# Kernel optimization log

Measured on AMD Instinct MI355X. Metric: run time of the kernel, lower is better.

## Reference

```python
import jax, jax.numpy as jnp
import numpy as np

B = 64          # graphs in batch
NVARS = 256     # variables per graph
LITS_PER = 2 * NVARS
NL = B * LITS_PER      # 32768 literals
CLS_PER = 1024
NC = B * CLS_PER       # 65536 clauses
K = 3                  # literals per clause (3-CNF)
D = 128
NUM_ITERS = 8


def setup_inputs() -> dict:
    key = jax.random.key(0)
    ks = jax.random.split(key, 16)
    # edge list of the sparse clause-literal incidence matrix adj_t [NC, NL]
    edge_clause = jnp.repeat(jnp.arange(NC, dtype=jnp.int32), K)            # [E]
    clause_graph = jnp.repeat(jnp.arange(NC, dtype=jnp.int32) // CLS_PER, K)
    lit_local = jax.random.randint(ks[0], (NC * K,), 0, LITS_PER, dtype=jnp.int32)
    edge_lit = clause_graph * LITS_PER + lit_local                          # [E]
    s = 0.05
    inp = {
        "edge_clause": edge_clause,
        "edge_lit": edge_lit,
        "x_l0": jax.random.uniform(ks[1], (NL, D), jnp.float32),
        "x_c0": jax.random.uniform(ks[2], (NC, D), jnp.float32),
        "W_ih_lc": jax.random.normal(ks[3], (D, D), jnp.float32) * s,
        "W_hh_lc": jax.random.normal(ks[4], (D, D), jnp.float32) * s,
        "b_ih_lc": jax.random.normal(ks[5], (D,), jnp.float32) * s,
        "b_hh_lc": jax.random.normal(ks[6], (D,), jnp.float32) * s,
        "W_ih_cl": jax.random.normal(ks[7], (D, 2 * D), jnp.float32) * s,
        "W_hh_cl": jax.random.normal(ks[8], (D, D), jnp.float32) * s,
        "b_ih_cl": jax.random.normal(ks[9], (D,), jnp.float32) * s,
        "b_hh_cl": jax.random.normal(ks[10], (D,), jnp.float32) * s,
        "L_vote_w": jax.random.normal(ks[11], (1, D), jnp.float32) * s,
        "L_vote_b": jax.random.normal(ks[12], (1,), jnp.float32) * s,
        "true_vec_w": jax.random.normal(ks[13], (1, D), jnp.float32) * s,
        "num_iters": NUM_ITERS,
    }
    return inp


def _l2norm(x):
    return x / jnp.linalg.norm(x, axis=1, keepdims=True)


def _rnn_cell(x, h, Wih, Whh, bih, bhh):
    # torch nn.RNN (tanh) single step: h' = tanh(x W_ih^T + b_ih + h W_hh^T + b_hh)
    return jnp.tanh(x @ Wih.T + bih + h @ Whh.T + bhh)


def _flip(x_l):
    # per graph, swap [pos vars | neg vars] halves
    return x_l.reshape(B, 2, NVARS, D)[:, ::-1].reshape(NL, D)


def reference(edge_clause, edge_lit, x_l0, x_c0,
              W_ih_lc, W_hh_lc, b_ih_lc, b_hh_lc,
              W_ih_cl, W_hh_cl, b_ih_cl, b_hh_cl,
              L_vote_w, L_vote_b, true_vec_w, num_iters):
    x_l = _l2norm(x_l0)
    x_c = _l2norm(x_c0)

    truth0 = x_l @ true_vec_w.T          # [NL, 1]
    clause0 = x_c                        # [NC, D]

    def step(carry, _):
        x_l, x_c = carry
        # LC: clause messages = adj_t @ x_l  (sparse matmul as gather+segment_sum)
        msg_c = jax.ops.segment_sum(x_l[edge_lit], edge_clause, num_segments=NC)
        x_c_new = _rnn_cell(msg_c, x_c, W_ih_lc, W_hh_lc, b_ih_lc, b_hh_lc)
        # CL: literal messages = adj_t^T @ x_c_new
        msg_l = jax.ops.segment_sum(x_c_new[edge_clause], edge_lit, num_segments=NL)
        inp = jnp.concatenate([msg_l, _flip(x_l)], axis=1)   # [NL, 2D]
        x_l_new = _rnn_cell(inp, x_l, W_ih_cl, W_hh_cl, b_ih_cl, b_hh_cl)
        x_l_n = _l2norm(x_l_new)
        x_c_n = _l2norm(x_c_new)
        truth = x_l_n @ true_vec_w.T                          # [NL, 1]
        return (x_l_n, x_c_n), (truth, x_c_n)

    (x_l, x_c), (truths, clauses) = jax.lax.scan(step, (x_l, x_c), None, length=num_iters)

    truth_all = jnp.concatenate([truth0[None], truths], axis=0)    # [T+1, NL, 1]
    clause_all = jnp.concatenate([clause0[None], clauses], axis=0)  # [T+1, NC, D]

    x_l_vote = x_l @ L_vote_w.T + L_vote_b                   # [NL, 1]
    vote_mean_pool = x_l_vote.reshape(B, LITS_PER, 1).mean(axis=1)  # [B, 1]

    # ragged per-graph lists in the original are contiguous blocks here;
    # we return the flat concatenations (identical data).
    return (x_l_vote, x_l, vote_mean_pool, truth_all[-1], truth_all, clause_all, truth_all[0])
```

## Files before the change

kernel.cpp:

```cpp
#include <hip/hip_runtime.h>
#include <math.h>

namespace {
constexpr int NVARS    = 256;
constexpr int LITS_PER = 2 * NVARS;
constexpr int Bg       = 64;
constexpr int NL       = Bg * LITS_PER;
constexpr int CLS_PER  = 1024;
constexpr int NC       = Bg * CLS_PER;
constexpr int NE       = NC * 3;
constexpr int D        = 128;
constexpr int T        = 8;

constexpr size_t OFF_VOTE  = 0;
constexpr size_t OFF_XL    = (size_t)NL;
constexpr size_t OFF_POOL  = OFF_XL + (size_t)NL * D;
constexpr size_t OFF_TLAST = OFF_POOL + Bg;
constexpr size_t OFF_TALL  = OFF_TLAST + NL;
constexpr size_t OFF_CALL  = OFF_TALL + (size_t)(T + 1) * NL;
constexpr size_t OFF_T0    = OFF_CALL + (size_t)(T + 1) * NC * D;

constexpr int PKM    = 16384;
constexpr int PK_TOT = 5 * PKM;
constexpr size_t SHM_LC = 2 * PKM * sizeof(unsigned short);
constexpr size_t SHM_CL = 2 * PKM * sizeof(unsigned short) + 1536;
}

typedef __attribute__((ext_vector_type(8))) short short8v;
typedef __attribute__((ext_vector_type(4))) float f32x4;

__device__ __forceinline__ unsigned short f2bf(float v) {
    unsigned u = __float_as_uint(v);
    return (unsigned short)((u + 0x7fffu + ((u >> 16) & 1u)) >> 16);
}
__device__ __forceinline__ float bf2f(unsigned short b) {
    return __uint_as_float(((unsigned)b) << 16);
}
__device__ __forceinline__ void cvt_frag(const float (&v)[8], short8v& ah, short8v& al) {
    #pragma unroll
    for (int j = 0; j < 8; j++) {
        unsigned short h = f2bf(v[j]);
        ah[j] = (short)h;
        al[j] = (short)f2bf(v[j] - bf2f(h));
    }
}
__device__ __forceinline__ float ftanh(float x) {
    float e = __builtin_amdgcn_exp2f(x * 2.885390081777926814f);
    return 1.0f - 2.0f * __builtin_amdgcn_rcpf(e + 1.0f);
}
__device__ __forceinline__ void mm2(f32x4& c, short8v ah, short8v al,
                                    const unsigned short* buf, int off) {
    short8v b = *(const short8v*)(buf + off);
    c = __builtin_amdgcn_mfma_f32_16x16x32_bf16(ah, b, c, 0, 0, 0);
    c = __builtin_amdgcn_mfma_f32_16x16x32_bf16(al, b, c, 0, 0, 0);
}
__device__ __forceinline__ void mm1(f32x4& c, short8v a,
                                    const unsigned short* buf, int off) {
    short8v b = *(const short8v*)(buf + off);
    c = __builtin_amdgcn_mfma_f32_16x16x32_bf16(a, b, c, 0, 0, 0);
}

__global__ __launch_bounds__(256) void pack5(
    const float* __restrict__ ihlc, const float* __restrict__ hhlc,
    const float* __restrict__ hhcl, const float* __restrict__ ihcl,
    unsigned short* __restrict__ pk) {
    int idx = blockIdx.x * 256 + threadIdx.x;
    int mat = idx >> 14, rel = idx & 16383;
    int j = rel & 7, lane = (rel >> 3) & 63, ks = (rel >> 9) & 3, n = rel >> 11;
    int r = n * 16 + (lane & 15);
    int k = ks * 32 + (lane >> 4) * 8 + j;
    float w;
    if (mat == 0)      w = ihlc[r * 128 + k];
    else if (mat == 1) w = hhlc[r * 128 + k];
    else if (mat == 2) w = hhcl[r * 128 + k];
    else if (mat == 3) w = ihcl[r * 256 + k];
    else               w = ihcl[r * 256 + 128 + k];
    pk[mat * PKM + rel] = f2bf(w);
}

__global__ void csr_count(const int* __restrict__ edge_lit, int* __restrict__ counts) {
    int e = blockIdx.x * blockDim.x + threadIdx.x;
    if (e < NE) atomicAdd(&counts[edge_lit[e]], 1);
}

__global__ __launch_bounds__(1024) void csr_scan(const int* __restrict__ counts,
                                                 int* __restrict__ offs,
                                                 int* __restrict__ cursor) {
    __shared__ int part[1024];
    const int t = threadIdx.x;
    const int base = t * 32;
    int local[32];
    int s = 0;
    for (int i = 0; i < 32; i++) { local[i] = s; s += counts[base + i]; }
    part[t] = s;
    __syncthreads();
    for (int d = 1; d < 1024; d <<= 1) {
        int v = 0;
        if (t >= d) v = part[t - d];
        __syncthreads();
        if (t >= d) part[t] += v;
        __syncthreads();
    }
    const int excl = (t == 0) ? 0 : part[t - 1];
    for (int i = 0; i < 32; i++) {
        int o = excl + local[i];
        offs[base + i] = o;
        cursor[base + i] = o;
    }
    if (t == 1023) offs[NL] = part[1023];
}

__global__ void csr_fill(const int* __restrict__ edge_lit, int* __restrict__ cursor,
                         int* __restrict__ csr) {
    int e = blockIdx.x * blockDim.x + threadIdx.x;
    if (e < NE) {
        int l = edge_lit[e];
        int p = atomicAdd(&cursor[l], 1);
        csr[p] = e / 3;
    }
}

__global__ void csr_sort(const int* __restrict__ offs, int* __restrict__ csr) {
    int l = blockIdx.x * blockDim.x + threadIdx.x;
    if (l >= NL) return;
    int s = offs[l], e = offs[l + 1];
    for (int i = s + 1; i < e; i++) {
        int v = csr[i];
        int j = i - 1;
        while (j >= s && csr[j] > v) { csr[j + 1] = csr[j]; j--; }
        csr[j + 1] = v;
    }
}

__global__ __launch_bounds__(64) void make_perm(const int* __restrict__ counts,
                                                int* __restrict__ perm) {
    __shared__ int d[64];
    const int b = blockIdx.x, i = threadIdx.x;
    d[i] = counts[b * 64 + i];
    __syncthreads();
    const int di = d[i];
    int rank = 0;
    for (int j = 0; j < 64; j++) {
        int dj = d[j];
        rank += (dj < di) || (dj == di && j < i);
    }
    perm[b * 64 + rank] = i;
}

__global__ void rownorm_dot(const float* __restrict__ in, float* __restrict__ out,
                            unsigned short* __restrict__ out_bf,
                            float* __restrict__ norms,
                            const float* __restrict__ dotw, float* __restrict__ dot0,
                            float* __restrict__ dot1, int nrows) {
    int wave = (int)((blockIdx.x * blockDim.x + threadIdx.x) >> 6);
    int lane = threadIdx.x & 63;
    if (wave >= nrows) return;
    const float* r = in + (size_t)wave * D;
    float v0 = r[lane], v1 = r[lane + 64];
    float ss = v0 * v0 + v1 * v1;
    #pragma unroll
    for (int m = 32; m; m >>= 1) ss += __shfl_xor(ss, m);
    float rn = 1.0f / sqrtf(ss);
    float y0 = v0 * rn, y1 = v1 * rn;
    float* o = out + (size_t)wave * D;
    o[lane] = y0;
    o[lane + 64] = y1;
    unsigned short* ob = out_bf + (size_t)wave * D;
    if (norms) {
        ob[lane] = f2bf(v0);
        ob[lane + 64] = f2bf(v1);
        if (lane == 0) norms[wave] = ss * rn;
    } else {
        ob[lane] = f2bf(y0);
        ob[lane + 64] = f2bf(y1);
    }
    if (dotw) {
        float dv = y0 * dotw[lane] + y1 * dotw[lane + 64];
        #pragma unroll
        for (int m = 32; m; m >>= 1) dv += __shfl_xor(dv, m);
        if (lane == 0) {
            dot0[wave] = dv;
            if (dot1) dot1[wave] = dv;
        }
    }
}

__device__ __forceinline__ void gather3b(const int* __restrict__ ep,
                                         const unsigned short* __restrict__ xlb,
                                         int arow, int g, float (&v)[4][8]) {
    int e0 = ep[3 * arow], e1 = ep[3 * arow + 1], e2 = ep[3 * arow + 2];
    const unsigned short* r0 = xlb + (size_t)e0 * D + g * 8;
    const unsigned short* r1 = xlb + (size_t)e1 * D + g * 8;
    const unsigned short* r2 = xlb + (size_t)e2 * D + g * 8;
    #pragma unroll
    for (int ks = 0; ks < 4; ks++) {
        short8v a = *(const short8v*)(r0 + ks * 32);
        short8v b = *(const short8v*)(r1 + ks * 32);
        short8v c = *(const short8v*)(r2 + ks * 32);
        #pragma unroll
        for (int j = 0; j < 8; j++)
            v[ks][j] = bf2f((unsigned short)a[j]) + bf2f((unsigned short)b[j]) +
                       bf2f((unsigned short)c[j]);
    }
}

__device__ __forceinline__ void gatherCSRb(const int* __restrict__ offs,
                                           const int* __restrict__ csr,
                                           const unsigned short* __restrict__ xcb,
                                           int arow, int g, float (&v)[4][8]) {
    #pragma unroll
    for (int ks = 0; ks < 4; ks++)
        #pragma unroll
        for (int j = 0; j < 8; j++) v[ks][j] = 0.f;
    const int s = offs[arow], e = offs[arow + 1];
    for (int p = s; p < e; p++) {
        const unsigned short* q = xcb + (size_t)csr[p] * D + g * 8;
        #pragma unroll
        for (int ks = 0; ks < 4; ks++) {
            short8v a = *(const short8v*)(q + ks * 32);
            #pragma unroll
            for (int j = 0; j < 8; j++) v[ks][j] += bf2f((unsigned short)a[j]);
        }
    }
}

__global__ __launch_bounds__(512, 4) void lc_mfma(
    const int* __restrict__ edge_lit, const unsigned short* __restrict__ xl_bf,
    unsigned short* xc_bf, float* norms,
    const unsigned short* __restrict__ pk,
    const float* __restrict__ bih, const float* __restrict__ bhh,
    float* __restrict__ xc_norm) {
    extern __shared__ __align__(16) unsigned short lds[];
    const int tid = threadIdx.x, wid = tid >> 6, lane = tid & 63;
    const int m = lane & 15, g = lane >> 4;
    const int p = blockIdx.x;
    const int blk = (p & 7) * 64 + (p >> 3);
    const int rowbase = blk * 128;
    const int arow = rowbase + wid * 16 + m;

    {
        const short8v* src = (const short8v*)pk;
        short8v* dst = (short8v*)lds;
        #pragma unroll
        for (int i = 0; i < 8; i++) dst[i * 512 + tid] = src[i * 512 + tid];
    }
    float v[4][8];
    gather3b(edge_lit, xl_bf, arow, g, v);
    short8v hvb[4];
    {
        const unsigned short* hr = xc_bf + (size_t)arow * D + g * 8;
        #pragma unroll
        for (int ks = 0; ks < 4; ks++) hvb[ks] = *(const short8v*)(hr + ks * 32);
    }
    const float rnh = __builtin_amdgcn_rcpf(norms[arow]);
    __syncthreads();

    short8v ah[4], al[4];
    #pragma unroll
    for (int ks = 0; ks < 4; ks++) cvt_frag(v[ks], ah[ks], al[ks]);

    f32x4 acc[8];
    #pragma unroll
    for (int n = 0; n < 8; n++) acc[n] = (f32x4)0.f;

    #pragma unroll
    for (int ks = 0; ks < 4; ks++)
        #pragma unroll
        for (int n = 0; n < 8; n++)
            mm2(acc[n], ah[ks], al[ks], lds, ((n * 4 + ks) * 64 + lane) * 8);

    float vh[4][8];
    #pragma unroll
    for (int ks = 0; ks < 4; ks++)
        #pragma unroll
        for (int j = 0; j < 8; j++)
            vh[ks][j] = bf2f((unsigned short)hvb[ks][j]) * rnh;
    #pragma unroll
    for (int ks = 0; ks < 4; ks++) cvt_frag(vh[ks], ah[ks], al[ks]);
    #pragma unroll
    for (int ks = 0; ks < 4; ks++)
        #pragma unroll
        for (int n = 0; n < 8; n++)
            mm2(acc[n], ah[ks], al[ks], lds + PKM, ((n * 4 + ks) * 64 + lane) * 8);

    float bias[8];
    #pragma unroll
    for (int n = 0; n < 8; n++) bias[n] = bih[n * 16 + m] + bhh[n * 16 + m];

    const int obase = rowbase + wid * 16 + g * 4;
    #pragma unroll
    for (int r = 0; r < 4; r++) {
        float w[8], ss = 0.f;
        #pragma unroll
        for (int n = 0; n < 8; n++) { w[n] = ftanh(acc[n][r] + bias[n]); ss += w[n] * w[n]; }
        ss += __shfl_xor(ss, 1); ss += __shfl_xor(ss, 2);
        ss += __shfl_xor(ss, 4); ss += __shfl_xor(ss, 8);
        const float rn = __builtin_amdgcn_rsqf(ss);
        const size_t rowoff = (size_t)(obase + r) * D + m;
        #pragma unroll
        for (int n = 0; n < 8; n++) {
            xc_norm[rowoff + n * 16] = w[n] * rn;
            xc_bf[rowoff + n * 16] = f2bf(w[n]);
        }
        if (m == 0) norms[obase + r] = ss * rn;
    }
}

__global__ __launch_bounds__(512, 4) void cl_mfma(
    const int* __restrict__ offs, const int* __restrict__ csr,
    const int* __restrict__ perm,
    const unsigned short* __restrict__ xc_bf,
    const unsigned short* __restrict__ xl_src,
    const unsigned short* __restrict__ pk,
    const float* __restrict__ bih, const float* __restrict__ bhh,
    const float* __restrict__ tv, const float* __restrict__ vw,
    const float* __restrict__ vb,
    unsigned short* __restrict__ xl_dst,
    float* __restrict__ xl_out,
    float* __restrict__ truth, float* __restrict__ truth2, float* __restrict__ vote) {
    extern __shared__ __align__(16) unsigned short lds[];
    float* scr = (float*)(lds + 2 * PKM);
    float* ssx = scr; float* twx = scr + 128; float* vwx = scr + 256;

    const int tid = threadIdx.x, wid = tid >> 6, lane = tid & 63;
    const int m = lane & 15, g = lane >> 4;
    const int rw = wid >> 1, nh = wid & 1, nbase = nh * 4;
    const int p0 = blockIdx.x;
    const int blk = (p0 & 7) * 64 + (p0 >> 3);
    const int lbase = blk * 64;
    const int arow = lbase + perm[lbase + rw * 16 + m];

    {
        const short8v* srcA = (const short8v*)(pk + 3 * PKM);
        const short8v* srcB = (const short8v*)(pk + 2 * PKM);
        short8v* d0 = (short8v*)lds;
        short8v* d1 = (short8v*)(lds + PKM);
        #pragma unroll
        for (int i = 0; i < 4; i++) d0[i * 512 + tid] = srcA[i * 512 + tid];
        #pragma unroll
        for (int i = 0; i < 4; i++) d1[i * 512 + tid] = srcB[i * 512 + tid];
    }
    float v[4][8];
    gatherCSRb(offs, csr, xc_bf, arow, g, v);
    short8v hv[4], fv[4];
    {
        const unsigned short* hr = xl_src + (size_t)arow * D + g * 8;
        const unsigned short* fp = xl_src + (size_t)(arow ^ 256) * D + g * 8;
        #pragma unroll
        for (int ks = 0; ks < 4; ks++) { hv[ks] = *(const short8v*)(hr + ks * 32);
                                         fv[ks] = *(const short8v*)(fp + ks * 32); }
    }
    __syncthreads();

    short8v ah[4], al[4];
    #pragma unroll
    for (int ks = 0; ks < 4; ks++) cvt_frag(v[ks], ah[ks], al[ks]);

    f32x4 acc[4];
    #pragma unroll
    for (int n = 0; n < 4; n++) acc[n] = (f32x4)0.f;

    short8v fr[4];
    {
        const short8v* srcF = (const short8v*)(pk + 4 * PKM);
        #pragma unroll
        for (int i = 0; i < 4; i++) fr[i] = srcF[i * 512 + tid];
    }

    #pragma unroll
    for (int ks = 0; ks < 4; ks++)
        #pragma unroll
        for (int nn = 0; nn < 4; nn++)
            mm2(acc[nn], ah[ks], al[ks], lds, (((nbase + nn) * 4 + ks) * 64 + lane) * 8);

    __syncthreads();
    {
        short8v* d0 = (short8v*)lds;
        #pragma unroll
        for (int i = 0; i < 4; i++) d0[i * 512 + tid] = fr[i];
    }
    #pragma unroll
    for (int ks = 0; ks < 4; ks++)
        #pragma unroll
        for (int nn = 0; nn < 4; nn++)
            mm1(acc[nn], hv[ks], lds + PKM, (((nbase + nn) * 4 + ks) * 64 + lane) * 8);

    __syncthreads();
    #pragma unroll
    for (int ks = 0; ks < 4; ks++)
        #pragma unroll
        for (int nn = 0; nn < 4; nn++)
            mm1(acc[nn], fv[ks], lds, (((nbase + nn) * 4 + ks) * 64 + lane) * 8);

    float bias[4], tvv[4], vwv[4];
    #pragma unroll
    for (int nn = 0; nn < 4; nn++) {
        int n = nbase + nn;
        bias[nn] = bih[n * 16 + m] + bhh[n * 16 + m];
        tvv[nn] = tv[n * 16 + m];
        vwv[nn] = vote ? vw[n * 16 + m] : 0.f;
    }
    float wv[4][4];
    #pragma unroll
    for (int r = 0; r < 4; r++) {
        float ssp = 0.f, twp = 0.f, vwp = 0.f;
        #pragma unroll
        for (int nn = 0; nn < 4; nn++) {
            float w = ftanh(acc[nn][r] + bias[nn]);
            wv[r][nn] = w;
            ssp += w * w; twp += w * tvv[nn]; vwp += w * vwv[nn];
        }
        ssp += __shfl_xor(ssp, 1); ssp += __shfl_xor(ssp, 2);
        ssp += __shfl_xor(ssp, 4); ssp += __shfl_xor(ssp, 8);
        twp += __shfl_xor(twp, 1); twp += __shfl_xor(twp, 2);
        twp += __shfl_xor(twp, 4); twp += __shfl_xor(twp, 8);
        if (vote) {
            vwp += __shfl_xor(vwp, 1); vwp += __shfl_xor(vwp, 2);
            vwp += __shfl_xor(vwp, 4); vwp += __shfl_xor(vwp, 8);
        }
        if (m == 0) {
            int rl = rw * 16 + g * 4 + r;
            ssx[rl * 2 + nh] = ssp;
            twx[rl * 2 + nh] = twp;
            if (vote) vwx[rl * 2 + nh] = vwp;
        }
    }
    __syncthreads();
    const float vb0 = vote ? vb[0] : 0.f;
    #pragma unroll
    for (int r = 0; r < 4; r++) {
        const int rl = rw * 16 + g * 4 + r;
        const int grow = lbase + perm[lbase + rl];
        const float ss = ssx[rl * 2] + ssx[rl * 2 + 1];
        const float rn = __builtin_amdgcn_rsqf(ss);
        const size_t rowoff = (size_t)grow * D + m;
        #pragma unroll
        for (int nn = 0; nn < 4; nn++) {
            const float y = wv[r][nn] * rn;
            xl_dst[rowoff + (nbase + nn) * 16] = f2bf(y);
            if (xl_out) xl_out[rowoff + (nbase + nn) * 16] = y;
        }
        if (m == 0 && nh == 0) {
            const float td = rn * (twx[rl * 2] + twx[rl * 2 + 1]);
            truth[grow] = td;
            if (truth2) truth2[grow] = td;
            if (vote) vote[grow] = rn * (vwx[rl * 2] + vwx[rl * 2 + 1]) + vb0;
        }
    }
}

__global__ void pool_kernel(const float* __restrict__ votes, float* __restrict__ pool) {
    __shared__ float s[4];
    int g = blockIdx.x, t = threadIdx.x;
    float v = votes[g * LITS_PER + t] + votes[g * LITS_PER + 256 + t];
    #pragma unroll
    for (int m = 32; m; m >>= 1) v += __shfl_xor(v, m);
    if ((t & 63) == 0) s[t >> 6] = v;
    __syncthreads();
    if (t == 0) pool[g] = (s[0] + s[1] + s[2] + s[3]) * (1.0f / LITS_PER);
}

extern "C" void kernel_launch(void* const* d_in, const int* in_sizes, int n_in,
                              void* d_out, int out_size, void* d_ws, size_t ws_size,
                              hipStream_t stream) {
    const int*   edge_lit = (const int*)d_in[1];
    const float* x_l0     = (const float*)d_in[2];
    const float* x_c0     = (const float*)d_in[3];
    const float* W_ih_lc  = (const float*)d_in[4];
    const float* W_hh_lc  = (const float*)d_in[5];
    const float* b_ih_lc  = (const float*)d_in[6];
    const float* b_hh_lc  = (const float*)d_in[7];
    const float* W_ih_cl  = (const float*)d_in[8];
    const float* W_hh_cl  = (const float*)d_in[9];
    const float* b_ih_cl  = (const float*)d_in[10];
    const float* b_hh_cl  = (const float*)d_in[11];
    const float* L_vote_w = (const float*)d_in[12];
    const float* L_vote_b = (const float*)d_in[13];
    const float* true_vec = (const float*)d_in[14];

    float* out   = (float*)d_out;
    float* xl_o  = out + OFF_XL;
    float* call  = out + OFF_CALL;
    float* tall  = out + OFF_TALL;

    unsigned short* xc_bf  = (unsigned short*)d_ws;
    unsigned short* xl_bf0 = xc_bf + (size_t)NC * D;
    unsigned short* xl_bf1 = xl_bf0 + (size_t)NL * D;
    unsigned short* pk     = xl_bf1 + (size_t)NL * D;
    float* norms = (float*)(pk + PK_TOT);
    int* counts = (int*)(norms + NC);
    int* offs   = counts + NL;
    int* cursor = offs + NL + 1;
    int* csr    = cursor + NL;
    int* perm   = csr + NE;

    hipMemsetAsync(counts, 0, NL * sizeof(int), stream);

    pack5<<<PK_TOT / 256, 256, 0, stream>>>(W_ih_lc, W_hh_lc, W_hh_cl, W_ih_cl, pk);
    csr_count<<<NE / 256, 256, 0, stream>>>(edge_lit, counts);
    csr_scan<<<1, 1024, 0, stream>>>(counts, offs, cursor);
    csr_fill<<<NE / 256, 256, 0, stream>>>(edge_lit, cursor, csr);
    csr_sort<<<NL / 256, 256, 0, stream>>>(offs, csr);
    make_perm<<<NL / 64, 64, 0, stream>>>(counts, perm);

    rownorm_dot<<<NL / 4, 256, 0, stream>>>(x_l0, xl_o, xl_bf0, nullptr, true_vec,
                                            tall, out + OFF_T0, NL);
    rownorm_dot<<<NC / 4, 256, 0, stream>>>(x_c0, call, xc_bf, norms, nullptr,
                                            nullptr, nullptr, NC);

    for (int t = 1; t <= T; t++) {
        const unsigned short* src = (t & 1) ? xl_bf0 : xl_bf1;
        unsigned short*       dst = (t & 1) ? xl_bf1 : xl_bf0;
        lc_mfma<<<NC / 128, 512, SHM_LC, stream>>>(
            edge_lit, src, xc_bf, norms, pk, b_ih_lc, b_hh_lc,
            call + (size_t)t * NC * D);
        cl_mfma<<<NL / 64, 512, SHM_CL, stream>>>(
            offs, csr, perm, xc_bf, src, pk,
            b_ih_cl, b_hh_cl, true_vec, L_vote_w, L_vote_b,
            dst, (t == T) ? xl_o : nullptr, tall + (size_t)t * NL,
            (t == T) ? out + OFF_TLAST : nullptr,
            (t == T) ? out + OFF_VOTE : nullptr);
    }

    pool_kernel<<<Bg, 256, 0, stream>>>(out + OFF_VOTE, out + OFF_POOL);
}
```

Measured before the change: 510.0 us.

## Split LC gather into per-edge bf16 MFMAs, stream outputs nontemporally, fuse init norms

In the LC kernel, the three gathered literal rows are no longer summed in fp32 and split into hi/lo bf16 parts. Each bf16 row now goes through its own single MFMA pass, using linearity so no split is needed, and the fp32 conversion work goes away. The CL kernel reads the final weight fragment directly from global memory instead of restaging it in LDS, which removes two block barriers. Large write-only outputs use nontemporal stores, and the two init normalization launches are merged into one kernel. The tradeoff is three MFMA passes instead of two for the gathered input, plus global-memory B-operand loads in CL.

```diff
diff --git a/kernel.cpp b/kernel.cpp
--- a/kernel.cpp
+++ b/kernel.cpp
@@ -59,6 +59,12 @@
     short8v b = *(const short8v*)(buf + off);
     c = __builtin_amdgcn_mfma_f32_16x16x32_bf16(a, b, c, 0, 0, 0);
 }
+__device__ __forceinline__ void mm1g(f32x4& c, short8v a,
+                                     const unsigned short* __restrict__ buf, int off) {
+    short8v b = *(const short8v*)(buf + off);
+    c = __builtin_amdgcn_mfma_f32_16x16x32_bf16(a, b, c, 0, 0, 0);
+}
+__device__ __forceinline__ void ntst(float* p, float v) { __builtin_nontemporal_store(v, p); }
 
 __global__ __launch_bounds__(256) void pack5(
     const float* __restrict__ ihlc, const float* __restrict__ hhlc,
@@ -147,60 +153,45 @@
     perm[b * 64 + rank] = i;
 }
 
-__global__ void rownorm_dot(const float* __restrict__ in, float* __restrict__ out,
-                            unsigned short* __restrict__ out_bf,
-                            float* __restrict__ norms,
-                            const float* __restrict__ dotw, float* __restrict__ dot0,
-                            float* __restrict__ dot1, int nrows) {
+__global__ void init_norm(const float* __restrict__ x_l0, const float* __restrict__ x_c0,
+                          float* __restrict__ xl_f32, unsigned short* __restrict__ xl_bf,
+                          float* __restrict__ xc_f32, unsigned short* __restrict__ xc_bf,
+                          float* __restrict__ norms,
+                          const float* __restrict__ tv, float* __restrict__ tall,
+                          float* __restrict__ t0) {
     int wave = (int)((blockIdx.x * blockDim.x + threadIdx.x) >> 6);
     int lane = threadIdx.x & 63;
-    if (wave >= nrows) return;
-    const float* r = in + (size_t)wave * D;
-    float v0 = r[lane], v1 = r[lane + 64];
-    float ss = v0 * v0 + v1 * v1;
-    #pragma unroll
-    for (int m = 32; m; m >>= 1) ss += __shfl_xor(ss, m);
-    float rn = 1.0f / sqrtf(ss);
-    float y0 = v0 * rn, y1 = v1 * rn;
-    float* o = out + (size_t)wave * D;
-    o[lane] = y0;
-    o[lane + 64] = y1;
-    unsigned short* ob = out_bf + (size_t)wave * D;
-    if (norms) {
+    if (wave < NL) {
+        const float* r = x_l0 + (size_t)wave * D;
+        float v0 = r[lane], v1 = r[lane + 64];
+        float ss = v0 * v0 + v1 * v1;
+        #pragma unroll
+        for (int m = 32; m; m >>= 1) ss += __shfl_xor(ss, m);
+        float rn = 1.0f / sqrtf(ss);
+        float y0 = v0 * rn, y1 = v1 * rn;
+        ntst(xl_f32 + (size_t)wave * D + lane, y0);
+        ntst(xl_f32 + (size_t)wave * D + lane + 64, y1);
+        unsigned short* ob = xl_bf + (size_t)wave * D;
+        ob[lane] = f2bf(y0);
+        ob[lane + 64] = f2bf(y1);
+        float dv = y0 * tv[lane] + y1 * tv[lane + 64];
+        #pragma unroll
+        for (int m = 32; m; m >>= 1) dv += __shfl_xor(dv, m);
+        if (lane == 0) { ntst(tall + wave, dv); ntst(t0 + wave, dv); }
+    } else if (wave < NL + NC) {
+        const int row = wave - NL;
+        const float* r = x_c0 + (size_t)row * D;
+        float v0 = r[lane], v1 = r[lane + 64];
+        float ss = v0 * v0 + v1 * v1;
+        #pragma unroll
+        for (int m = 32; m; m >>= 1) ss += __shfl_xor(ss, m);
+        float rn = 1.0f / sqrtf(ss);
+        ntst(xc_f32 + (size_t)row * D + lane, v0 * rn);
+        ntst(xc_f32 + (size_t)row * D + lane + 64, v1 * rn);
+        unsigned short* ob = xc_bf + (size_t)row * D;
         ob[lane] = f2bf(v0);
         ob[lane + 64] = f2bf(v1);
-        if (lane == 0) norms[wave] = ss * rn;
-    } else {
-        ob[lane] = f2bf(y0);
-        ob[lane + 64] = f2bf(y1);
-    }
-    if (dotw) {
-        float dv = y0 * dotw[lane] + y1 * dotw[lane + 64];
-        #pragma unroll
-        for (int m = 32; m; m >>= 1) dv += __shfl_xor(dv, m);
-        if (lane == 0) {
-            dot0[wave] = dv;
-            if (dot1) dot1[wave] = dv;
-        }
-    }
-}
-
-__device__ __forceinline__ void gather3b(const int* __restrict__ ep,
-                                         const unsigned short* __restrict__ xlb,
-                                         int arow, int g, float (&v)[4][8]) {
-    int e0 = ep[3 * arow], e1 = ep[3 * arow + 1], e2 = ep[3 * arow + 2];
-    const unsigned short* r0 = xlb + (size_t)e0 * D + g * 8;
-    const unsigned short* r1 = xlb + (size_t)e1 * D + g * 8;
-    const unsigned short* r2 = xlb + (size_t)e2 * D + g * 8;
-    #pragma unroll
-    for (int ks = 0; ks < 4; ks++) {
-        short8v a = *(const short8v*)(r0 + ks * 32);
-        short8v b = *(const short8v*)(r1 + ks * 32);
-        short8v c = *(const short8v*)(r2 + ks * 32);
-        #pragma unroll
-        for (int j = 0; j < 8; j++)
-            v[ks][j] = bf2f((unsigned short)a[j]) + bf2f((unsigned short)b[j]) +
-                       bf2f((unsigned short)c[j]);
+        if (lane == 0) norms[row] = ss * rn;
     }
 }
 
@@ -244,8 +235,17 @@
         #pragma unroll
         for (int i = 0; i < 8; i++) dst[i * 512 + tid] = src[i * 512 + tid];
     }
-    float v[4][8];
-    gather3b(edge_lit, xl_bf, arow, g, v);
+    const int e0 = edge_lit[3 * arow], e1 = edge_lit[3 * arow + 1], e2 = edge_lit[3 * arow + 2];
+    const unsigned short* r0 = xl_bf + (size_t)e0 * D + g * 8;
+    const unsigned short* r1 = xl_bf + (size_t)e1 * D + g * 8;
+    const unsigned short* r2 = xl_bf + (size_t)e2 * D + g * 8;
+    short8v aA[4], aB[4], aC[4];
+    #pragma unroll
+    for (int ks = 0; ks < 4; ks++) aA[ks] = *(const short8v*)(r0 + ks * 32);
+    #pragma unroll
+    for (int ks = 0; ks < 4; ks++) aB[ks] = *(const short8v*)(r1 + ks * 32);
+    #pragma unroll
+    for (int ks = 0; ks < 4; ks++) aC[ks] = *(const short8v*)(r2 + ks * 32);
     short8v hvb[4];
     {
         const unsigned short* hr = xc_bf + (size_t)arow * D + g * 8;
@@ -255,10 +255,6 @@
     const float rnh = __builtin_amdgcn_rcpf(norms[arow]);
     __syncthreads();
 
-    short8v ah[4], al[4];
-    #pragma unroll
-    for (int ks = 0; ks < 4; ks++) cvt_frag(v[ks], ah[ks], al[ks]);
-
     f32x4 acc[8];
     #pragma unroll
     for (int n = 0; n < 8; n++) acc[n] = (f32x4)0.f;
@@ -267,21 +263,34 @@
     for (int ks = 0; ks < 4; ks++)
         #pragma unroll
         for (int n = 0; n < 8; n++)
-            mm2(acc[n], ah[ks], al[ks], lds, ((n * 4 + ks) * 64 + lane) * 8);
-
-    float vh[4][8];
-    #pragma unroll
-    for (int ks = 0; ks < 4; ks++)
-        #pragma unroll
-        for (int j = 0; j < 8; j++)
-            vh[ks][j] = bf2f((unsigned short)hvb[ks][j]) * rnh;
-    #pragma unroll
-    for (int ks = 0; ks < 4; ks++) cvt_frag(vh[ks], ah[ks], al[ks]);
+            mm1(acc[n], aA[ks], lds, ((n * 4 + ks) * 64 + lane) * 8);
     #pragma unroll
     for (int ks = 0; ks < 4; ks++)
         #pragma unroll
         for (int n = 0; n < 8; n++)
-            mm2(acc[n], ah[ks], al[ks], lds + PKM, ((n * 4 + ks) * 64 + lane) * 8);
+            mm1(acc[n], aB[ks], lds, ((n * 4 + ks) * 64 + lane) * 8);
+    #pragma unroll
+    for (int ks = 0; ks < 4; ks++)
+        #pragma unroll
+        for (int n = 0; n < 8; n++)
+            mm1(acc[n], aC[ks], lds, ((n * 4 + ks) * 64 + lane) * 8);
+
+    {
+        float vh[4][8];
+        #pragma unroll
+        for (int ks = 0; ks < 4; ks++)
+            #pragma unroll
+            for (int j = 0; j < 8; j++)
+                vh[ks][j] = bf2f((unsigned short)hvb[ks][j]) * rnh;
+        short8v ah[4], al[4];
+        #pragma unroll
+        for (int ks = 0; ks < 4; ks++) cvt_frag(vh[ks], ah[ks], al[ks]);
+        #pragma unroll
+        for (int ks = 0; ks < 4; ks++)
+            #pragma unroll
+            for (int n = 0; n < 8; n++)
+                mm2(acc[n], ah[ks], al[ks], lds + PKM, ((n * 4 + ks) * 64 + lane) * 8);
+    }
 
     float bias[8];
     #pragma unroll
@@ -299,7 +308,7 @@
         const size_t rowoff = (size_t)(obase + r) * D + m;
         #pragma unroll
         for (int n = 0; n < 8; n++) {
-            xc_norm[rowoff + n * 16] = w[n] * rn;
+            ntst(xc_norm + rowoff + n * 16, w[n] * rn);
             xc_bf[rowoff + n * 16] = f2bf(w[n]);
         }
         if (m == 0) norms[obase + r] = ss * rn;
@@ -360,37 +369,24 @@
     #pragma unroll
     for (int n = 0; n < 4; n++) acc[n] = (f32x4)0.f;
 
-    short8v fr[4];
-    {
-        const short8v* srcF = (const short8v*)(pk + 4 * PKM);
-        #pragma unroll
-        for (int i = 0; i < 4; i++) fr[i] = srcF[i * 512 + tid];
-    }
-
     #pragma unroll
     for (int ks = 0; ks < 4; ks++)
         #pragma unroll
         for (int nn = 0; nn < 4; nn++)
             mm2(acc[nn], ah[ks], al[ks], lds, (((nbase + nn) * 4 + ks) * 64 + lane) * 8);
 
-    __syncthreads();
-    {
-        short8v* d0 = (short8v*)lds;
-        #pragma unroll
-        for (int i = 0; i < 4; i++) d0[i * 512 + tid] = fr[i];
-    }
     #pragma unroll
     for (int ks = 0; ks < 4; ks++)
         #pragma unroll
         for (int nn = 0; nn < 4; nn++)
             mm1(acc[nn], hv[ks], lds + PKM, (((nbase + nn) * 4 + ks) * 64 + lane) * 8);
 
-    __syncthreads();
+    const unsigned short* pkF = pk + 4 * PKM;
     #pragma unroll
     for (int ks = 0; ks < 4; ks++)
         #pragma unroll
         for (int nn = 0; nn < 4; nn++)
-            mm1(acc[nn], fv[ks], lds, (((nbase + nn) * 4 + ks) * 64 + lane) * 8);
+            mm1g(acc[nn], fv[ks], pkF, (((nbase + nn) * 4 + ks) * 64 + lane) * 8);
 
     float bias[4], tvv[4], vwv[4];
     #pragma unroll
@@ -438,13 +434,13 @@
         for (int nn = 0; nn < 4; nn++) {
             const float y = wv[r][nn] * rn;
             xl_dst[rowoff + (nbase + nn) * 16] = f2bf(y);
-            if (xl_out) xl_out[rowoff + (nbase + nn) * 16] = y;
+            if (xl_out) ntst(xl_out + rowoff + (nbase + nn) * 16, y);
         }
         if (m == 0 && nh == 0) {
             const float td = rn * (twx[rl * 2] + twx[rl * 2 + 1]);
-            truth[grow] = td;
-            if (truth2) truth2[grow] = td;
-            if (vote) vote[grow] = rn * (vwx[rl * 2] + vwx[rl * 2 + 1]) + vb0;
+            ntst(truth + grow, td);
+            if (truth2) ntst(truth2 + grow, td);
+            if (vote) ntst(vote + grow, rn * (vwx[rl * 2] + vwx[rl * 2 + 1]) + vb0);
         }
     }
 }
@@ -503,10 +499,9 @@
     csr_sort<<<NL / 256, 256, 0, stream>>>(offs, csr);
     make_perm<<<NL / 64, 64, 0, stream>>>(counts, perm);
 
-    rownorm_dot<<<NL / 4, 256, 0, stream>>>(x_l0, xl_o, xl_bf0, nullptr, true_vec,
-                                            tall, out + OFF_T0, NL);
-    rownorm_dot<<<NC / 4, 256, 0, stream>>>(x_c0, call, xc_bf, norms, nullptr,
-                                            nullptr, nullptr, NC);
+    init_norm<<<(NL + NC) / 4, 256, 0, stream>>>(
+        x_l0, x_c0, xl_o, xl_bf0, call, xc_bf, norms,
+        true_vec, tall, out + OFF_T0);
 
     for (int t = 1; t <= T; t++) {
         const unsigned short* src = (t & 1) ? xl_bf0 : xl_bf1;
```

Measured after the change: 851.3 us. +66.9%, slower.
